# Kernel tuning notes

Measured on AMD Instinct MI355X. Metric: run time of the kernel, lower is better.

Reference implementation:

```python
import jax, jax.numpy as jnp
import numpy as np

C = 192
DCT = 7
EPS = 1e-5
LOW_X = [0,0,1,1,0,2,2,1,2,0,3,4,0,1,3,0,1,2,3,4,5,0,1,2,3,4,5,6,1,2,3,4]
LOW_Y = [0,1,0,1,2,0,1,2,2,3,0,0,4,3,1,5,4,3,2,1,0,6,5,4,3,2,1,0,6,5,4,3]


def _dct_basis():
    # basis[i, tx, ty] = bf(tx, ux_i, DCT) * bf(ty, vy_i, DCT)
    t = jnp.arange(DCT, dtype=jnp.float32)
    fx = jnp.array(LOW_X, dtype=jnp.float32)  # mapper scale = dct_h//7 = 1
    fy = jnp.array(LOW_Y, dtype=jnp.float32)
    def bf(freq):
        r = jnp.cos(jnp.pi * freq[:, None] * (t[None, :] + 0.5) / DCT) / jnp.sqrt(jnp.float32(DCT))
        return jnp.where(freq[:, None] == 0, r, r * jnp.sqrt(jnp.float32(2.0)))
    bx, by = bf(fx), bf(fy)  # [32, 7] each
    return bx[:, :, None] * by[:, None, :]  # [32, 7, 7]


def reference(x, wg1, bn2_g, bn2_b, bn2_m, bn2_v, wg2, bg2, beta, w1d, b1d, bn1_g, bn1_b, bn1_m, bn1_v):
    n, c, h, w = x.shape
    # gate: 1x1 conv -> BN2d (eval) -> ReLU -> global avg pool -> 1x1 conv
    g = jnp.einsum('nchw,oc->nohw', x, wg1)
    g = (g - bn2_m[None, :, None, None]) * (bn2_g / jnp.sqrt(bn2_v + EPS))[None, :, None, None] + bn2_b[None, :, None, None]
    g = jax.nn.relu(g).mean(axis=(2, 3))          # [n, 32]
    xg = g @ wg2.T + bg2                           # [n, 32]
    xg = jax.nn.relu(jnp.tanh(xg)) + beta          # gate_ac + beta
    # data-dependent channel partition from batch element 0 (torch uses .item() -> detached)
    xg0 = jax.lax.stop_gradient(xg[0])
    s = xg0.sum()
    p_mid = jnp.round(xg0[:31] / s * c)            # param[1..31]
    param = jnp.concatenate([jnp.zeros(1, jnp.float32), p_mid,
                             (jnp.float32(c) - p_mid.sum())[None]])  # [33]
    # build DCT filter: slice param[i]:param[i+1] gets basis i, later i overwrites
    ch = jnp.arange(c, dtype=jnp.float32)
    basis = _dct_basis()                           # [32, 7, 7]
    filt = jnp.zeros((c, DCT, DCT), jnp.float32)
    for i in range(32):
        m = (ch >= param[i]) & (ch < param[i + 1])
        filt = jnp.where(m[:, None, None], basis[i], filt)
    xp = x.reshape(n, c, DCT, h // DCT, DCT, w // DCT).mean(axis=(3, 5))
    y = jnp.sum(xp * filt[None], axis=(2, 3))      # [n, c] weighted spatial pooling
    # Conv1d(c, c, k=3, pad=1) on length-1 sequence: only center tap w1d[:, :, 1]
    y = y @ w1d[:, :, 1].T + b1d
    y = (y - bn1_m) * (bn1_g / jnp.sqrt(bn1_v + EPS)) + bn1_b
    y = jax.nn.relu(y)
    return x * y[:, :, None, None] + x


def setup_inputs() -> dict:
    key = jax.random.key(0)
    ks = jax.random.split(key, 16)
    n, h, w = 64, 56, 56
    return {
        'x':     jax.random.normal(ks[0], (n, C, h, w), jnp.float32),
        'wg1':   jax.random.normal(ks[1], (32, C), jnp.float32) * (2.0 / C) ** 0.5,
        'bn2_g': jax.random.uniform(ks[2], (32,), jnp.float32, 0.8, 1.2),
        'bn2_b': jax.random.normal(ks[3], (32,), jnp.float32) * 0.1,
        'bn2_m': jax.random.normal(ks[4], (32,), jnp.float32) * 0.1,
        'bn2_v': jax.random.uniform(ks[5], (32,), jnp.float32, 0.5, 1.5),
        'wg2':   jax.random.normal(ks[6], (32, 32), jnp.float32) * (2.0 / 32) ** 0.5,
        'bg2':   jax.random.normal(ks[7], (32,), jnp.float32) * 0.1,
        'beta':  jax.random.uniform(ks[8], (1,), jnp.float32, 0.05, 0.25),
        'w1d':   jax.random.normal(ks[9], (C, C, 3), jnp.float32) * (2.0 / (3 * C)) ** 0.5,
        'b1d':   jax.random.normal(ks[10], (C,), jnp.float32) * 0.1,
        'bn1_g': jax.random.uniform(ks[11], (C,), jnp.float32, 0.8, 1.2),
        'bn1_b': jax.random.normal(ks[12], (C,), jnp.float32) * 0.1,
        'bn1_m': jax.random.normal(ks[13], (C,), jnp.float32) * 0.1,
        'bn1_v': jax.random.uniform(ks[14], (C,), jnp.float32, 0.5, 1.5),
    }
```

## Files before the change

kernel.cpp:

```cpp
#include <hip/hip_runtime.h>
#include <hip/hip_bf16.h>
#include <math.h>

#define CCH 192
#define EPS 1e-5f

typedef float vfloat4 __attribute__((ext_vector_type(4)));

__device__ __constant__ int d_LOWX[32] = {0,0,1,1,0,2,2,1,2,0,3,4,0,1,3,0,1,2,3,4,5,0,1,2,3,4,5,6,1,2,3,4};
__device__ __constant__ int d_LOWY[32] = {0,1,0,1,2,0,1,2,2,3,0,0,4,3,1,5,4,3,2,1,0,6,5,4,3,2,1,0,6,5,4,3};

#define GLOAD4(dst, addr) \
  asm volatile("global_load_dwordx4 %0, %1, off" : "=v"(dst) : "v"(addr))
#define GLOAD1(dst, addr) \
  asm volatile("global_load_dword %0, %1, off" : "=v"(dst) : "v"(addr))
#define VMWAIT(n) do { \
  asm volatile("s_waitcnt vmcnt(" #n ")" ::: "memory"); \
  __builtin_amdgcn_sched_barrier(0); \
} while (0)

#define ISSUE(buf, base) do { \
  _Pragma("unroll") \
  for (int g = 0; g < 7; ++g) { \
    GLOAD4(buf[2 * g],     (base) + g * 112 + lidx); \
    GLOAD4(buf[2 * g + 1], (base) + g * 112 + 56 + lidx); \
  } \
} while (0)

#define REDUCE(buf, res) do { \
  _Pragma("unroll") \
  for (int g = 0; g < 7; ++g) { \
    float s = (buf[2*g].x + buf[2*g].y + buf[2*g].z + buf[2*g].w) + \
              (buf[2*g+1].x + buf[2*g+1].y + buf[2*g+1].z + buf[2*g+1].w); \
    s = act ? s : 0.f; \
    float a = s + __shfl_xor(s, 1); \
    a += __shfl(a, l + 28); \
    a += __shfl(a, l + 14); \
    res[g] = a; \
  } \
} while (0)

__global__ __launch_bounds__(256) void fused_pre_kernel(
    const float* __restrict__ x, const float* __restrict__ w1d,
    const float* __restrict__ wg1,
    const float* __restrict__ bn2_g, const float* __restrict__ bn2_b,
    const float* __restrict__ bn2_m, const float* __restrict__ bn2_v,
    float* __restrict__ xp, float* __restrict__ wt, float* __restrict__ partial) {
  const int b = blockIdx.x;
  const int t = threadIdx.x;
  if (b >= 200) {
    const int ub = b - 200;
    const int n = ub / 12;
    const int q0 = (ub % 12) * 4;
    const int wv = t >> 6, l = t & 63;
    const bool act = l < 56;
    const int lidx = act ? l : 0;
    const vfloat4* xb = (const vfloat4*)(x + (size_t)n * CCH * 3136 + (size_t)wv * 3136);
    const vfloat4* base0 = xb + (size_t)(q0 + 0) * 4 * 784;
    const vfloat4* base1 = xb + (size_t)(q0 + 1) * 4 * 784;
    const vfloat4* base2 = xb + (size_t)(q0 + 2) * 4 * 784;
    const vfloat4* base3 = xb + (size_t)(q0 + 3) * 4 * 784;
    vfloat4 A[14], B[14];
    float r0[7], r1[7], r2[7], r3[7];
    ISSUE(A, base0);
    ISSUE(B, base1);
    VMWAIT(14);
    REDUCE(A, r0);
    ISSUE(A, base2);
    VMWAIT(14);
    REDUCE(B, r1);
    ISSUE(B, base3);
    VMWAIT(14);
    REDUCE(A, r2);
    VMWAIT(0);
    REDUCE(B, r3);
    if (act && l < 14 && (l & 1) == 0) {
      const int cb = l >> 1;
      float* d0 = xp + ((size_t)n * CCH + (q0 + 0) * 4 + wv) * 49 + cb;
      float* d1 = xp + ((size_t)n * CCH + (q0 + 1) * 4 + wv) * 49 + cb;
      float* d2 = xp + ((size_t)n * CCH + (q0 + 2) * 4 + wv) * 49 + cb;
      float* d3 = xp + ((size_t)n * CCH + (q0 + 3) * 4 + wv) * 49 + cb;
#pragma unroll
      for (int g = 0; g < 7; ++g) {
        d0[g * 7] = r0[g] * (1.f / 64.f);
        d1[g * 7] = r1[g] * (1.f / 64.f);
        d2[g * 7] = r2[g] * (1.f / 64.f);
        d3[g * 7] = r3[g] * (1.f / 64.f);
      }
    }
  } else if (b >= 56) {
    const int i = (b - 56) * 256 + t;
    const int cc = i / CCH, k = i - cc * CCH;
    wt[k * CCH + cc] = w1d[cc * (CCH * 3) + 3 * k + 1];
  } else {
    const int h = b;
    const int wv = t >> 6, w = t & 63;
    float acc[8];
#pragma unroll
    for (int o = 0; o < 8; ++o) acc[o] = 0.f;
    const float* xrow = x + h * 56;
    for (int cc0 = 0; cc0 < CCH; cc0 += 8) {
      float xq[8];
#pragma unroll
      for (int j = 0; j < 8; ++j)
        GLOAD1(xq[j], xrow + (size_t)(cc0 + j) * 3136 + ((w < 56) ? w : 0));
      VMWAIT(0);
#pragma unroll
      for (int j = 0; j < 8; ++j) {
        float xvv = (w < 56) ? xq[j] : 0.f;
#pragma unroll
        for (int o = 0; o < 8; ++o)
          acc[o] += xvv * wg1[(wv * 8 + o) * CCH + cc0 + j];
      }
    }
#pragma unroll
    for (int o = 0; o < 8; ++o) {
      const int oo = wv * 8 + o;
      float sc = bn2_g[oo] * rsqrtf(bn2_v[oo] + EPS);
      float v = acc[o] * sc + (bn2_b[oo] - bn2_m[oo] * sc);
      v = (w < 56) ? fmaxf(v, 0.f) : 0.f;
#pragma unroll
      for (int s = 1; s < 64; s <<= 1) v += __shfl_xor(v, s);
      if (w == 0) partial[h * 32 + oo] = v;
    }
  }
}

__global__ __launch_bounds__(256) void scale_kernel(
    const float* __restrict__ partial, const float* __restrict__ wg2,
    const float* __restrict__ bg2, const float* __restrict__ beta,
    const float* __restrict__ xp, const float* __restrict__ wt,
    const float* __restrict__ b1d,
    const float* __restrict__ bn1_g, const float* __restrict__ bn1_b,
    const float* __restrict__ bn1_m, const float* __restrict__ bn1_v,
    float* __restrict__ scale) {
  __shared__ float gm[32];
  __shared__ float xg[32];
  __shared__ float param[33];
  __shared__ float Btab[49];
  __shared__ float yl[CCH];
  const int n = blockIdx.x, t = threadIdx.x;
  if (t < 32) {
    float s = 0.f;
    for (int hh = 0; hh < 56; ++hh) s += partial[hh * 32 + t];
    gm[t] = s * (1.f / 3136.f);
  }
  if (t < 49) {
    int f = t / 7, tt = t % 7;
    float r = cosf(3.14159265358979323846f * (float)f * ((float)tt + 0.5f) / 7.f) * rsqrtf(7.f);
    Btab[t] = (f == 0) ? r : r * sqrtf(2.f);
  }
  __syncthreads();
  if (t < 32) {
    float a = bg2[t];
    for (int k = 0; k < 32; ++k) a += gm[k] * wg2[t * 32 + k];
    xg[t] = fmaxf(tanhf(a), 0.f) + beta[0];
  }
  __syncthreads();
  if (t == 0) {
    float s = 0.f;
    for (int k = 0; k < 32; ++k) s += xg[k];
    float psum = 0.f;
    param[0] = 0.f;
    for (int i = 0; i < 31; ++i) {
      float p = rintf(xg[i] / s * (float)CCH);
      param[i + 1] = p;
      psum += p;
    }
    param[32] = (float)CCH - psum;
  }
  __syncthreads();
  if (t < CCH) {
    int bi = -1;
    float cf = (float)t;
    for (int i = 0; i < 32; ++i)
      if (cf >= param[i] && cf < param[i + 1]) bi = i;
    int fx = (bi >= 0) ? d_LOWX[bi] : 0;
    int fy = (bi >= 0) ? d_LOWY[bi] : 0;
    const float* xc = xp + ((size_t)n * CCH + t) * 49;
    float s = 0.f;
    for (int cell = 0; cell < 49; ++cell) {
      int a = cell / 7, bb = cell - a * 7;
      float w = Btab[fx * 7 + a] * Btab[fy * 7 + bb];
      s += xc[cell] * ((bi >= 0) ? w : 0.f);
    }
    yl[t] = s;
  }
  __syncthreads();
  if (t < CCH) {
    float acc = b1d[t];
#pragma unroll 8
    for (int k = 0; k < CCH; ++k) acc += yl[k] * wt[k * CCH + t];
    float sc = bn1_g[t] * rsqrtf(bn1_v[t] + EPS);
    float v = (acc - bn1_m[t]) * sc + bn1_b[t];
    scale[n * CCH + t] = 1.f + fmaxf(v, 0.f);
  }
}

__global__ __launch_bounds__(256) void apply_kernel(
    const float* __restrict__ x, const float* __restrict__ scale,
    float* __restrict__ out) {
  const int base = blockIdx.x * 2048 + threadIdx.x;
  const vfloat4* __restrict__ xv = (const vfloat4*)x;
  vfloat4* __restrict__ ov = (vfloat4*)out;
  vfloat4 vv[8];
  float sj[8];
#pragma unroll
  for (int k = 0; k < 8; ++k) {
    const int f = base + k * 256;
    GLOAD4(vv[k], xv + f);
    GLOAD1(sj[k], scale + f / 784);
  }
  VMWAIT(0);
#pragma unroll
  for (int k = 0; k < 8; ++k) {
    const int f = base + k * 256;
    ov[f] = vv[k] * sj[k];
  }
}

extern "C" void kernel_launch(void* const* d_in, const int* in_sizes, int n_in,
                              void* d_out, int out_size, void* d_ws, size_t ws_size,
                              hipStream_t stream) {
  const float* x     = (const float*)d_in[0];
  const float* wg1   = (const float*)d_in[1];
  const float* bn2_g = (const float*)d_in[2];
  const float* bn2_b = (const float*)d_in[3];
  const float* bn2_m = (const float*)d_in[4];
  const float* bn2_v = (const float*)d_in[5];
  const float* wg2   = (const float*)d_in[6];
  const float* bg2   = (const float*)d_in[7];
  const float* beta  = (const float*)d_in[8];
  const float* w1d   = (const float*)d_in[9];
  const float* b1d   = (const float*)d_in[10];
  const float* bn1_g = (const float*)d_in[11];
  const float* bn1_b = (const float*)d_in[12];
  const float* bn1_m = (const float*)d_in[13];
  const float* bn1_v = (const float*)d_in[14];
  float* out = (float*)d_out;

  float* ws      = (float*)d_ws;
  float* partial = ws;
  float* filt    = partial + 1792;
  float* wt      = filt + 9408;
  float* xp      = wt + 36864;
  float* scale   = xp + 602112;

  fused_pre_kernel<<<968, 256, 0, stream>>>(x, w1d, wg1, bn2_g, bn2_b, bn2_m, bn2_v,
                                            xp, wt, partial);
  scale_kernel<<<64, 256, 0, stream>>>(partial, wg2, bg2, beta, xp, wt, b1d,
                                       bn1_g, bn1_b, bn1_m, bn1_v, scale);
  apply_kernel<<<4704, 256, 0, stream>>>(x, scale, out);
}
```

Before: 340.2 us.

## Fuse scale computation into apply kernel with per-batch quarter blocks

Merges the scale and apply kernels into one launch. Each of 256 blocks recomputes the per-batch channel scale into shared memory, then scales a quarter of that batch's activations. This removes one kernel launch and the global scale buffer round trip. In exchange it does four times the redundant gate and conv1d work, and the streaming pass runs on far fewer blocks with a serial setup phase before any loads start.

After: 339.8 us. About the same (-0.1%).

```diff
diff --git a/kernel.cpp b/kernel.cpp
--- a/kernel.cpp
+++ b/kernel.cpp
@@ -126,20 +126,22 @@
   }
 }
 
-__global__ __launch_bounds__(256) void scale_kernel(
+__global__ __launch_bounds__(256) void scale_apply_kernel(
     const float* __restrict__ partial, const float* __restrict__ wg2,
     const float* __restrict__ bg2, const float* __restrict__ beta,
     const float* __restrict__ xp, const float* __restrict__ wt,
     const float* __restrict__ b1d,
     const float* __restrict__ bn1_g, const float* __restrict__ bn1_b,
     const float* __restrict__ bn1_m, const float* __restrict__ bn1_v,
-    float* __restrict__ scale) {
+    const float* __restrict__ x, float* __restrict__ out) {
   __shared__ float gm[32];
   __shared__ float xg[32];
   __shared__ float param[33];
   __shared__ float Btab[49];
   __shared__ float yl[CCH];
-  const int n = blockIdx.x, t = threadIdx.x;
+  __shared__ float sl[CCH];
+  const int blk = blockIdx.x, t = threadIdx.x;
+  const int n = blk >> 2, qi = blk & 3;
   if (t < 32) {
     float s = 0.f;
     for (int hh = 0; hh < 56; ++hh) s += partial[hh * 32 + t];
@@ -193,29 +195,28 @@
     for (int k = 0; k < CCH; ++k) acc += yl[k] * wt[k * CCH + t];
     float sc = bn1_g[t] * rsqrtf(bn1_v[t] + EPS);
     float v = (acc - bn1_m[t]) * sc + bn1_b[t];
-    scale[n * CCH + t] = 1.f + fmaxf(v, 0.f);
-  }
-}
-
-__global__ __launch_bounds__(256) void apply_kernel(
-    const float* __restrict__ x, const float* __restrict__ scale,
-    float* __restrict__ out) {
-  const int base = blockIdx.x * 2048 + threadIdx.x;
+    sl[t] = 1.f + fmaxf(v, 0.f);
+  }
+  __syncthreads();
   const vfloat4* __restrict__ xv = (const vfloat4*)x;
   vfloat4* __restrict__ ov = (vfloat4*)out;
-  vfloat4 vv[8];
-  float sj[8];
-#pragma unroll
-  for (int k = 0; k < 8; ++k) {
-    const int f = base + k * 256;
-    GLOAD4(vv[k], xv + f);
-    GLOAD1(sj[k], scale + f / 784);
-  }
-  VMWAIT(0);
-#pragma unroll
-  for (int k = 0; k < 8; ++k) {
-    const int f = base + k * 256;
-    ov[f] = vv[k] * sj[k];
+  const int off0 = qi * 37632 + t;
+  const size_t base = (size_t)n * 150528 + off0;
+#pragma unroll
+  for (int B = 0; B < 18; ++B) {
+    vfloat4 vv[8];
+#pragma unroll
+    for (int j = 0; j < 8; ++j) vv[j] = xv[base + (B * 8 + j) * 256];
+#pragma unroll
+    for (int j = 0; j < 8; ++j) {
+      const int off = off0 + (B * 8 + j) * 256;
+      ov[base + (B * 8 + j) * 256] = vv[j] * sl[off / 784];
+    }
+  }
+#pragma unroll
+  for (int k = 144; k < 147; ++k) {
+    const int off = off0 + k * 256;
+    ov[base + k * 256] = xv[base + k * 256] * sl[off / 784];
   }
 }
 
@@ -244,11 +245,9 @@
   float* filt    = partial + 1792;
   float* wt      = filt + 9408;
   float* xp      = wt + 36864;
-  float* scale   = xp + 602112;
 
   fused_pre_kernel<<<968, 256, 0, stream>>>(x, w1d, wg1, bn2_g, bn2_b, bn2_m, bn2_v,
                                             xp, wt, partial);
-  scale_kernel<<<64, 256, 0, stream>>>(partial, wg2, bg2, beta, xp, wt, b1d,
-                                       bn1_g, bn1_b, bn1_m, bn1_v, scale);
-  apply_kernel<<<4704, 256, 0, stream>>>(x, scale, out);
+  scale_apply_kernel<<<256, 256, 0, stream>>>(partial, wg2, bg2, beta, xp, wt, b1d,
+                                              bn1_g, bn1_b, bn1_m, bn1_v, x, out);
 }
```
